# Optimization experiments

Hardware: AMD Instinct MI355X
Metric: run time of the kernel (lower is better)

The kernel has to match this reference:

```python
import jax, jax.numpy as jnp
import numpy as np

R_MIN = 0.01
R_MAX = 0.6
H = 32            # polar radial bins (after pooling)
W = 64            # polar angular bins (after pooling)
UP_R = 10         # radial upsampling factor
UP_T = 10         # angular upsampling factor
ATT_ALPHA = 5.0
B, C, IMG = 64, 3, 224


def _conv(x, w, b):
    # NCHW valid conv, stride 1 (matches nn.Conv2d default padding=0)
    y = jax.lax.conv_general_dilated(x, w, (1, 1), 'VALID',
                                     dimension_numbers=('NCHW', 'OIHW', 'NCHW'))
    return y + b[None, :, None, None]


def _maxpool2(x):
    return jax.lax.reduce_window(x, -jnp.inf, jax.lax.max,
                                 (1, 1, 2, 2), (1, 1, 2, 2), 'VALID')


def _grid_sample_border(x, grid):
    # F.grid_sample, bilinear, padding_mode='border', align_corners=False
    Bn, Cn, Hi, Wi = x.shape
    ix = ((grid[..., 0] + 1.0) * Wi - 1.0) * 0.5   # x-coord -> width index
    iy = ((grid[..., 1] + 1.0) * Hi - 1.0) * 0.5   # y-coord -> height index
    x0f = jnp.floor(ix)
    y0f = jnp.floor(iy)
    wx = (ix - x0f)[..., None]
    wy = (iy - y0f)[..., None]
    x0 = jnp.clip(x0f.astype(jnp.int32), 0, Wi - 1)
    x1 = jnp.clip(x0f.astype(jnp.int32) + 1, 0, Wi - 1)
    y0 = jnp.clip(y0f.astype(jnp.int32), 0, Hi - 1)
    y1 = jnp.clip(y0f.astype(jnp.int32) + 1, 0, Hi - 1)
    bidx = jnp.arange(Bn)[:, None, None]
    v00 = x[bidx, :, y0, x0]   # [B,Hg,Wg,C]
    v01 = x[bidx, :, y0, x1]
    v10 = x[bidx, :, y1, x0]
    v11 = x[bidx, :, y1, x1]
    out = (v00 * (1 - wx) * (1 - wy) + v01 * wx * (1 - wy)
           + v10 * (1 - wx) * wy + v11 * wx * wy)
    return jnp.transpose(out, (0, 3, 1, 2))  # [B,C,Hg,Wg]


def setup_inputs() -> dict:
    key = jax.random.key(0)
    ks = jax.random.split(key, 10)
    x = jax.random.normal(ks[0], (B, C, IMG, IMG), dtype=jnp.float32)
    l_t_prev = jax.random.uniform(ks[1], (B, 2), dtype=jnp.float32)
    conv1_w = jax.random.normal(ks[2], (6, C, 5, 5), dtype=jnp.float32) * 0.1
    conv1_b = jnp.zeros((6,), jnp.float32)
    conv2_w = jax.random.normal(ks[3], (16, 6, 5, 5), dtype=jnp.float32) * 0.1
    conv2_b = jnp.zeros((16,), jnp.float32)
    fc1_w = jax.random.normal(ks[4], (8, 16), dtype=jnp.float32) * 0.1
    fc1_b = jnp.zeros((8,), jnp.float32)
    fc2_w = jax.random.normal(ks[5], (2, 8), dtype=jnp.float32) * 0.1
    fc2_b = jnp.zeros((2,), jnp.float32)
    return dict(x=x, l_t_prev=l_t_prev, conv1_w=conv1_w, conv1_b=conv1_b,
                conv2_w=conv2_w, conv2_b=conv2_b, fc1_w=fc1_w, fc1_b=fc1_b,
                fc2_w=fc2_w, fc2_b=fc2_b)


def reference(x, l_t_prev, conv1_w, conv1_b, conv2_w, conv2_b,
              fc1_w, fc1_b, fc2_w, fc2_b):
    # --- attention branch: conv -> maxpool -> conv -> GAP -> fc -> sigmoid ---
    h = _conv(x, conv1_w, conv1_b)
    h = _maxpool2(h)
    h = _conv(h, conv2_w, conv2_b)
    feat = h.mean(axis=(2, 3))                     # AdaptiveAvgPool2d(1), [B,16]
    h = jax.nn.relu(feat @ fc1_w.T + fc1_b)
    weight = jax.nn.sigmoid(h @ fc2_w.T + fc2_b) * ATT_ALPHA   # [B,2]
    # --- per-batch log-polar grid ---
    Hg, Wg = H * UP_R, W * UP_T
    angle = 2.0 * jnp.pi * jnp.arange(Wg, dtype=jnp.float32) / Wg
    unit = jnp.stack([jnp.sin(angle), jnp.cos(angle)], axis=-1)   # [Wg,2]
    start = jnp.log(R_MIN * weight[:, 0])
    stop = jnp.log(R_MAX * weight[:, 1])
    t = jnp.arange(Hg, dtype=jnp.float32) / (Hg - 1)
    radii = jnp.exp(start[:, None] + (stop - start)[:, None] * t[None])  # [B,Hg]
    grid = radii[:, :, None, None] * unit[None, None]     # [B,Hg,Wg,2]
    grid = grid + l_t_prev[:, None, None, :]
    # --- irregular bilinear sampling + box filter ---
    sampled = _grid_sample_border(x, grid)                 # [B,C,Hg,Wg]
    Bn, Cn = sampled.shape[:2]
    pooled = sampled.reshape(Bn, Cn, H, UP_R, W, UP_T).mean(axis=(3, 5))
    return pooled, weight
```

## Files before the change

kernel.cpp:

```cpp
#include <hip/hip_runtime.h>
#include <math.h>

#define Bn    64
#define Cn    3
#define IMG   224
#define PLANE (IMG*IMG)
#define C1    6
#define P1    110
#define NVALID (106*106)
#define Hh    32
#define Ww    64
#define UPR   10
#define UPT   10
#define Hg    (Hh*UPR)
#define Wg    (Ww*UPT)
#define POOLED_SIZE (Bn*Cn*Hh*Ww)
#define NCHUNK 28
#define PSTRIDE 152
#define ROWB  (IMG*8)
#define TPB1  448

typedef unsigned short u16;
typedef unsigned long long ull;
typedef _Float16 h8v __attribute__((ext_vector_type(8)));
typedef float f4v __attribute__((ext_vector_type(4)));

#define PART_FLOATS ((size_t)Bn * NCHUNK * PSTRIDE)
#define X4B_U16     ((size_t)Bn * PLANE * 4)
#define WS_NEEDED   ((PART_FLOATS + Bn * 2) * 4 + X4B_U16 * 2)

__device__ __forceinline__ unsigned hpack(float a, float b) {
    union { _Float16 h; u16 u; } x, y;
    x.h = (_Float16)a; y.h = (_Float16)b;
    return (unsigned)x.u | ((unsigned)y.u << 16);
}
__device__ __forceinline__ float h2lo(unsigned v) {
    union { _Float16 h; u16 u; } c; c.u = (u16)(v & 0xffffu); return (float)c.h;
}
__device__ __forceinline__ float h2hi(unsigned v) {
    union { _Float16 h; u16 u; } c; c.u = (u16)(v >> 16); return (float)c.h;
}

#define GSHFL(v, idx) __shfl((v), (lane & 48) + (idx), 64)

__global__ __launch_bounds__(TPB1) void k1_fused(
    const float* __restrict__ x,
    const float* __restrict__ w1,
    const float* __restrict__ b1,
    float* __restrict__ partial,
    u16* __restrict__ x4h,
    int do_pack)
{
    __shared__ __attribute__((aligned(16))) unsigned char xs[12 * ROWB + 128];
    __shared__ __attribute__((aligned(16))) _Float16 sa[5][64][8];
    __shared__ float rowR[7][C1][4];
    __shared__ float edgeLo[4][C1][4];
    __shared__ float edgeHi[4][C1][4];

    const int b     = blockIdx.x;
    const int chunk = blockIdx.y;
    const int tid   = threadIdx.x;
    const int wid   = tid >> 6;
    const int lane  = tid & 63;
    const int n     = lane & 15;
    const int g     = lane >> 4;
    const int gy0   = chunk * 8;

    const float* xb = x + (size_t)b * (Cn * PLANE);
    u16* ob = x4h + (size_t)b * PLANE * 4;

    if (wid == 0) {
        #pragma unroll
        for (int ky = 0; ky < 5; ++ky) {
            #pragma unroll
            for (int j = 0; j < 8; ++j) {
                const int kmem = g * 8 + j;
                const int ic = kmem & 3, kx = kmem >> 2;
                float w = 0.0f;
                if (n < C1 && ic < 3 && kx < 5)
                    w = w1[((n * 3 + ic) * 5 + ky) * 5 + kx];
                sa[ky][lane][j] = (_Float16)w;
            }
        }
    } else {
        for (int i = tid - 64; i < 12 * 112; i += TPB1 - 64) {
            const int r = i / 112;
            const int p = i - r * 112;
            const int gy = gy0 + r;
            uint4 U; U.x = U.y = U.z = U.w = 0u;
            if (gy < IMG) {
                const float2 v0 = *(const float2*)(xb + 0 * PLANE + gy * IMG + 2 * p);
                const float2 v1 = *(const float2*)(xb + 1 * PLANE + gy * IMG + 2 * p);
                const float2 v2 = *(const float2*)(xb + 2 * PLANE + gy * IMG + 2 * p);
                U.x = hpack(v0.x, v1.x);
                U.y = hpack(v2.x, 0.0f);
                U.z = hpack(v0.y, v1.y);
                U.w = hpack(v2.y, 0.0f);
            }
            *(uint4*)(xs + r * ROWB + p * 16) = U;
            if (do_pack && r < 8)
                *(uint4*)(ob + ((size_t)gy * IMG + 2 * p) * 4) = U;
        }
    }
    __syncthreads();

    h8v a[5];
    #pragma unroll
    for (int ky = 0; ky < 5; ++ky) a[ky] = *(const h8v*)&sa[ky][lane][0];
    f4v binit;
    #pragma unroll
    for (int e = 0; e < 4; ++e) {
        const int oc = g * 4 + e;
        binit[e] = (oc < C1) ? b1[oc] : 0.0f;
    }

    float colsum[4][4];
    #pragma unroll
    for (int py = 0; py < 4; ++py)
        #pragma unroll
        for (int e = 0; e < 4; ++e) colsum[py][e] = 0.0f;

    #pragma unroll
    for (int si = 0; si < 2; ++si) {
        const int s = wid * 2 + si;
        const unsigned sByte = (unsigned)(s * 128 + n * 8 + g * 16);

        f4v acc[8];
        #pragma unroll
        for (int q = 0; q < 8; ++q) acc[q] = binit;

        #pragma unroll
        for (int r = 0; r < 12; ++r) {
            h8v bf;
            const unsigned char* bp = xs + r * ROWB + sByte;
            ((ull*)&bf)[0] = *(const ull*)bp;
            ((ull*)&bf)[1] = *(const ull*)(bp + 8);
            #pragma unroll
            for (int ky = 0; ky < 5; ++ky) {
                const int q = r - ky;
                if (q >= 0 && q < 8)
                    acc[q] = __builtin_amdgcn_mfma_f32_16x16x32_f16(
                        a[ky], bf, acc[q], 0, 0, 0);
            }
        }

        #pragma unroll
        for (int py = 0; py < 4; ++py) {
            #pragma unroll
            for (int e = 0; e < 4; ++e) {
                float t = fmaxf(acc[2 * py][e], acc[2 * py + 1][e]);
                t = fmaxf(t, __shfl_xor(t, 1, 64));
                if (s == 13 && n >= 12) t = 0.0f;
                colsum[py][e] += t;
                const int oc = g * 4 + e;
                if (s == 0) {
                    const float c0 = GSHFL(t, 0), c1 = GSHFL(t, 2);
                    const float c2 = GSHFL(t, 4), c3 = GSHFL(t, 6);
                    const float S1 = c0, S2 = S1 + c1, S3 = S2 + c2, S4 = S3 + c3;
                    const float sv = (n == 0) ? S1 : (n == 1) ? S2 : (n == 2) ? S3 : S4;
                    if (n < 4 && oc < C1) edgeLo[py][oc][n] = sv;
                }
                if (s == 13) {
                    const float d109 = GSHFL(t, 10), d108 = GSHFL(t, 8);
                    const float d107 = GSHFL(t, 6),  d106 = GSHFL(t, 4);
                    const float U1 = d109, U2 = U1 + d108, U3 = U2 + d107, U4 = U3 + d106;
                    const float uv = (n == 0) ? U1 : (n == 1) ? U2 : (n == 2) ? U3 : U4;
                    if (n < 4 && oc < C1) edgeHi[py][oc][n] = uv;
                }
            }
        }
    }

    #pragma unroll
    for (int py = 0; py < 4; ++py) {
        #pragma unroll
        for (int e = 0; e < 4; ++e) {
            float v = colsum[py][e];
            v += __shfl_xor(v, 2, 64);
            v += __shfl_xor(v, 4, 64);
            v += __shfl_xor(v, 8, 64);
            const int oc = g * 4 + e;
            if (n == 0 && oc < C1) rowR[wid][oc][py] = v;
        }
    }
    __syncthreads();

    if (tid < 150) {
        const int oc = tid / 25;
        const int rem = tid - oc * 25;
        const int ky = rem / 5, kx = rem - ky * 5;
        float total = 0.0f;
        #pragma unroll
        for (int py = 0; py < 4; ++py) {
            const int y = chunk * 4 + py;
            const bool valid = (y < P1) && ((unsigned)(y - ky) <= 105u);
            float v = rowR[0][oc][py] + rowR[1][oc][py] + rowR[2][oc][py]
                    + rowR[3][oc][py] + rowR[4][oc][py] + rowR[5][oc][py]
                    + rowR[6][oc][py];
            if (kx > 0) v -= edgeLo[py][oc][kx - 1];
            if (kx < 4) v -= edgeHi[py][oc][3 - kx];
            total += valid ? v : 0.0f;
        }
        partial[((size_t)b * NCHUNK + chunk) * PSTRIDE + tid] = total;
    }
}

__global__ __launch_bounds__(256) void k2_head(
    const float* __restrict__ partial, const float* __restrict__ w2,
    const float* __restrict__ b2, const float* __restrict__ fc1w,
    const float* __restrict__ fc1b, const float* __restrict__ fc2w,
    const float* __restrict__ fc2b, float* __restrict__ wt_ws,
    float* __restrict__ out)
{
    const int b = blockIdx.x;
    const int tid = threadIdx.x;
    __shared__ float wsb[150];
    __shared__ float sfeat[16];
    __shared__ float sh[8];

    if (tid < 150) {
        const float* p = partial + (size_t)b * NCHUNK * PSTRIDE + tid;
        float s = 0.0f;
        #pragma unroll
        for (int c = 0; c < NCHUNK; ++c) s += p[c * PSTRIDE];
        wsb[tid] = s;
    }
    __syncthreads();
    if (tid < 16) {
        float s = 0.0f;
        for (int j = 0; j < 150; ++j) s += w2[tid * 150 + j] * wsb[j];
        sfeat[tid] = b2[tid] + s * (1.0f / (float)NVALID);
    }
    __syncthreads();
    if (tid < 8) {
        float s = fc1b[tid];
        #pragma unroll
        for (int j = 0; j < 16; ++j) s += fc1w[tid * 16 + j] * sfeat[j];
        sh[tid] = fmaxf(s, 0.0f);
    }
    __syncthreads();
    if (tid < 2) {
        float s = fc2b[tid];
        #pragma unroll
        for (int j = 0; j < 8; ++j) s += fc2w[tid * 8 + j] * sh[j];
        float sig = (s >= 0.0f) ? (1.0f / (1.0f + expf(-s)))
                                : (expf(s) / (1.0f + expf(s)));
        const float wgt = 5.0f * sig;
        wt_ws[b * 2 + tid] = wgt;
        out[POOLED_SIZE + b * 2 + tid] = wgt;
    }
}

__device__ __forceinline__ void sample_coords(
    float gxn, float gyn, int& x0, int& y0, float& wx, float& wy)
{
    float ix = ((gxn + 1.0f) * (float)IMG - 1.0f) * 0.5f;
    float iy = ((gyn + 1.0f) * (float)IMG - 1.0f) * 0.5f;
    ix = fminf(fmaxf(ix, 0.0f), (float)(IMG - 1));
    iy = fminf(fmaxf(iy, 0.0f), (float)(IMG - 1));
    x0 = (int)ix; if (x0 > IMG - 2) x0 = IMG - 2;
    y0 = (int)iy; if (y0 > IMG - 2) y0 = IMG - 2;
    wx = ix - (float)x0;
    wy = iy - (float)y0;
}

__global__ __launch_bounds__(640) void k3_fused_head(
    const u16* __restrict__ x4h,
    const float* __restrict__ ltp,
    const float* __restrict__ partial,
    const float* __restrict__ w2,  const float* __restrict__ b2,
    const float* __restrict__ fc1w, const float* __restrict__ fc1b,
    const float* __restrict__ fc2w, const float* __restrict__ fc2b,
    float* __restrict__ out)
{
    __shared__ float part[3 * Wg];
    __shared__ float wsb[152];
    __shared__ float sfp[16][10];
    __shared__ float sfeat[16];
    __shared__ float sh[8];
    __shared__ float sWt[2];

    const int L = blockIdx.x;
    const int q = L >> 3;
    const int h = q & 31;
    const int b = (L & 7) + 8 * (q >> 5);
    const int tid = threadIdx.x;

    if (tid < 150) {
        const float* p = partial + (size_t)b * NCHUNK * PSTRIDE + tid;
        float s = 0.0f;
        #pragma unroll
        for (int c = 0; c < NCHUNK; ++c) s += p[c * PSTRIDE];
        wsb[tid] = s;
    }
    __syncthreads();
    if (tid < 160) {
        const int oc = tid / 10, gq = tid - (tid / 10) * 10;
        float s = 0.0f;
        #pragma unroll
        for (int j = 0; j < 15; ++j)
            s += w2[oc * 150 + gq * 15 + j] * wsb[gq * 15 + j];
        sfp[oc][gq] = s;
    }
    __syncthreads();
    if (tid < 16) {
        float s = 0.0f;
        #pragma unroll
        for (int g2 = 0; g2 < 10; ++g2) s += sfp[tid][g2];
        sfeat[tid] = b2[tid] + s * (1.0f / (float)NVALID);
    }
    __syncthreads();
    if (tid < 8) {
        float s = fc1b[tid];
        #pragma unroll
        for (int j = 0; j < 16; ++j) s += fc1w[tid * 16 + j] * sfeat[j];
        sh[tid] = fmaxf(s, 0.0f);
    }
    __syncthreads();
    if (tid < 2) {
        float s = fc2b[tid];
        #pragma unroll
        for (int j = 0; j < 8; ++j) s += fc2w[tid * 8 + j] * sh[j];
        const float sig = (s >= 0.0f) ? (1.0f / (1.0f + expf(-s)))
                                      : (expf(s) / (1.0f + expf(s)));
        const float wgt = 5.0f * sig;
        sWt[tid] = wgt;
        if (h == 0) out[POOLED_SIZE + b * 2 + tid] = wgt;
    }
    __syncthreads();

    const float w0 = sWt[0];
    const float w1 = sWt[1];
    const float l0 = ltp[b * 2 + 0];
    const float l1 = ltp[b * 2 + 1];
    const float start = logf(0.01f * w0);
    const float stop  = logf(0.6f  * w1);
    const float dr = stop - start;

    const float angle = 6.283185307179586f * (float)tid / (float)Wg;
    const float sn = __sinf(angle);
    const float cs = __cosf(angle);

    const u16* xb4 = x4h + (size_t)b * PLANE * 4;

    int xi[UPR], yi[UPR];
    float wxa[UPR], wya[UPR];
    #pragma unroll
    for (int i = 0; i < UPR; ++i) {
        const float ri = __expf(start + dr * ((float)(h * UPR + i)
                                              * (1.0f / (float)(Hg - 1))));
        sample_coords(ri * sn + l0, ri * cs + l1, xi[i], yi[i], wxa[i], wya[i]);
    }

    float acc0 = 0.0f, acc1 = 0.0f, acc2 = 0.0f;
    #pragma unroll
    for (int bb = 0; bb < 2; ++bb) {
        uint4 R0[5], R1[5];
        #pragma unroll
        for (int i = 0; i < 5; ++i) {
            const int s = bb * 5 + i;
            const u16* base = xb4 + ((size_t)(yi[s] * IMG + xi[s])) * 4;
            R0[i] = *(const uint4*)(base);
            R1[i] = *(const uint4*)(base + IMG * 4);
        }
        #pragma unroll
        for (int i = 0; i < 5; ++i) {
            const int s = bb * 5 + i;
            const float wx = wxa[s], wy = wya[s];
            const float wx0 = 1.0f - wx, wy0 = 1.0f - wy;
            const float w00 = wx0 * wy0, w01 = wx * wy0;
            const float w10 = wx0 * wy,  w11 = wx * wy;
            acc0 += w00*h2lo(R0[i].x) + w01*h2lo(R0[i].z)
                  + w10*h2lo(R1[i].x) + w11*h2lo(R1[i].z);
            acc1 += w00*h2hi(R0[i].x) + w01*h2hi(R0[i].z)
                  + w10*h2hi(R1[i].x) + w11*h2hi(R1[i].z);
            acc2 += w00*h2lo(R0[i].y) + w01*h2lo(R0[i].w)
                  + w10*h2lo(R1[i].y) + w11*h2lo(R1[i].w);
        }
    }
    part[0 * Wg + tid] = acc0;
    part[1 * Wg + tid] = acc1;
    part[2 * Wg + tid] = acc2;
    __syncthreads();

    if (tid < Cn * Ww) {
        const int c = tid / Ww;
        const int w = tid % Ww;
        const float* p = part + c * Wg + w * UPT;
        float s = 0.0f;
        #pragma unroll
        for (int j = 0; j < UPT; ++j) s += p[j];
        out[(((size_t)b * Cn + c) * Hh + h) * Ww + w] = s * (1.0f / (UPR * UPT));
    }
}

__global__ __launch_bounds__(640) void k3_sample_pool_nchw(
    const float* __restrict__ x, const float* __restrict__ ltp,
    const float* __restrict__ wt, float* __restrict__ out)
{
    __shared__ float part[3 * Wg];
    const int L = blockIdx.x;
    const int q = L >> 3;
    const int h = q & 31;
    const int b = (L & 7) + 8 * (q >> 5);
    const int tid = threadIdx.x;

    const float w0 = wt[b * 2 + 0];
    const float w1 = wt[b * 2 + 1];
    const float l0 = ltp[b * 2 + 0];
    const float l1 = ltp[b * 2 + 1];
    const float start = logf(0.01f * w0);
    const float stop  = logf(0.6f  * w1);
    const float dr = stop - start;
    const float angle = 6.283185307179586f * (float)tid / (float)Wg;
    const float sn = __sinf(angle);
    const float cs = __cosf(angle);
    const float* xb = x + (size_t)b * Cn * PLANE;

    float acc0 = 0.0f, acc1 = 0.0f, acc2 = 0.0f;
    #pragma unroll
    for (int i = 0; i < UPR; ++i) {
        const float ri = __expf(start + dr * ((float)(h * UPR + i)
                                              * (1.0f / (float)(Hg - 1))));
        int x0, y0; float wx, wy;
        sample_coords(ri * sn + l0, ri * cs + l1, x0, y0, wx, wy);
        const float wx0 = 1.0f - wx, wy0 = 1.0f - wy;
        const float w00 = wx0 * wy0, w01 = wx * wy0;
        const float w10 = wx0 * wy,  w11 = wx * wy;
        const int o00 = y0 * IMG + x0;
        acc0 += w00*xb[o00] + w01*xb[o00+1] + w10*xb[o00+IMG] + w11*xb[o00+IMG+1];
        const float* x1p = xb + PLANE;
        acc1 += w00*x1p[o00] + w01*x1p[o00+1] + w10*x1p[o00+IMG] + w11*x1p[o00+IMG+1];
        const float* x2p = xb + 2 * PLANE;
        acc2 += w00*x2p[o00] + w01*x2p[o00+1] + w10*x2p[o00+IMG] + w11*x2p[o00+IMG+1];
    }
    part[0 * Wg + tid] = acc0;
    part[1 * Wg + tid] = acc1;
    part[2 * Wg + tid] = acc2;
    __syncthreads();

    if (tid < Cn * Ww) {
        const int c = tid / Ww;
        const int w = tid % Ww;
        const float* p = part + c * Wg + w * UPT;
        float s = 0.0f;
        #pragma unroll
        for (int j = 0; j < UPT; ++j) s += p[j];
        out[(((size_t)b * Cn + c) * Hh + h) * Ww + w] = s * (1.0f / (UPR * UPT));
    }
}

extern "C" void kernel_launch(void* const* d_in, const int* in_sizes, int n_in,
                              void* d_out, int out_size, void* d_ws, size_t ws_size,
                              hipStream_t stream) {
    const float* x       = (const float*)d_in[0];
    const float* ltp     = (const float*)d_in[1];
    const float* conv1_w = (const float*)d_in[2];
    const float* conv1_b = (const float*)d_in[3];
    const float* conv2_w = (const float*)d_in[4];
    const float* conv2_b = (const float*)d_in[5];
    const float* fc1_w   = (const float*)d_in[6];
    const float* fc1_b   = (const float*)d_in[7];
    const float* fc2_w   = (const float*)d_in[8];
    const float* fc2_b   = (const float*)d_in[9];
    float* out = (float*)d_out;

    const int do_pack = (ws_size >= WS_NEEDED) ? 1 : 0;

    float* part_ws = (float*)d_ws;
    float* wt_ws   = part_ws + PART_FLOATS;
    u16*   x4h     = (u16*)(wt_ws + Bn * 2);

    k1_fused<<<dim3(Bn, NCHUNK), dim3(TPB1), 0, stream>>>(
        x, conv1_w, conv1_b, part_ws, x4h, do_pack);

    if (do_pack) {
        k3_fused_head<<<dim3(Hh * Bn), dim3(Wg), 0, stream>>>(
            x4h, ltp, part_ws, conv2_w, conv2_b,
            fc1_w, fc1_b, fc2_w, fc2_b, out);
    } else {
        k2_head<<<dim3(Bn), dim3(256), 0, stream>>>(part_ws, conv2_w, conv2_b,
                                                    fc1_w, fc1_b, fc2_w, fc2_b,
                                                    wt_ws, out);
        k3_sample_pool_nchw<<<dim3(Hh * Bn), dim3(Wg), 0, stream>>>(
            x, ltp, wt_ws, out);
    }
}
```

Baseline: 174.3 us.

## Split conv1 into small 2D-tiled single-wave blocks with atomic accumulation

Replaces the 448-thread per-row-chunk conv kernel with 64-thread blocks that each own a 16x16 spatial tile (14x14 tiles per image), staging the fp16-packed tile in a small shared buffer. Per-block window sums are accumulated into a single per-batch buffer with atomicAdd, so the head kernels no longer reduce over 28 partial chunks. A new single-block prep kernel builds the fp16 MFMA weight fragments once and zeroes the accumulator. The aim is more parallelism and less shared memory per block. The cost is an extra launch, halo rows loaded twice by neighbouring tiles, atomic contention, and float summation order that is no longer deterministic.

```diff
diff --git a/kernel.cpp b/kernel.cpp
--- a/kernel.cpp
+++ b/kernel.cpp
@@ -15,24 +15,29 @@
 #define Hg    (Hh*UPR)
 #define Wg    (Ww*UPT)
 #define POOLED_SIZE (Bn*Cn*Hh*Ww)
-#define NCHUNK 28
-#define PSTRIDE 152
-#define ROWB  (IMG*8)
-#define TPB1  448
+#define WSTRIDE 152
+
+#define NSTRIP 14
+#define NCP    14
+#define NBLK1  (NSTRIP*NCP*Bn)
+#define XROW   24
+#define NROW   20
 
 typedef unsigned short u16;
 typedef unsigned long long ull;
 typedef _Float16 h8v __attribute__((ext_vector_type(8)));
 typedef float f4v __attribute__((ext_vector_type(4)));
 
-#define PART_FLOATS ((size_t)Bn * NCHUNK * PSTRIDE)
-#define X4B_U16     ((size_t)Bn * PLANE * 4)
-#define WS_NEEDED   ((PART_FLOATS + Bn * 2) * 4 + X4B_U16 * 2)
-
-__device__ __forceinline__ unsigned hpack(float a, float b) {
-    union { _Float16 h; u16 u; } x, y;
-    x.h = (_Float16)a; y.h = (_Float16)b;
-    return (unsigned)x.u | ((unsigned)y.u << 16);
+#define WSUM_F   ((size_t)Bn * WSTRIDE)
+#define WT_OFF   WSUM_F
+#define AF_OFF_F (WSUM_F + Bn*2)
+#define AF_U16   (5*64*8)
+#define X4H_OFF_F (AF_OFF_F + AF_U16/2)
+#define X4B_U16  ((size_t)Bn * PLANE * 4)
+#define WS_NEEDED ((size_t)X4H_OFF_F * 4 + X4B_U16 * 2)
+
+__device__ __forceinline__ u16 f16b(float f) {
+    union { _Float16 h; u16 u; } c; c.h = (_Float16)f; return c.u;
 }
 __device__ __forceinline__ float h2lo(unsigned v) {
     union { _Float16 h; u16 u; } c; c.u = (u16)(v & 0xffffu); return (float)c.h;
@@ -43,87 +48,98 @@
 
 #define GSHFL(v, idx) __shfl((v), (lane & 48) + (idx), 64)
 
-__global__ __launch_bounds__(TPB1) void k1_fused(
-    const float* __restrict__ x,
-    const float* __restrict__ w1,
-    const float* __restrict__ b1,
-    float* __restrict__ partial,
-    u16* __restrict__ x4h,
-    int do_pack)
-{
-    __shared__ __attribute__((aligned(16))) unsigned char xs[12 * ROWB + 128];
-    __shared__ __attribute__((aligned(16))) _Float16 sa[5][64][8];
-    __shared__ float rowR[7][C1][4];
-    __shared__ float edgeLo[4][C1][4];
-    __shared__ float edgeHi[4][C1][4];
-
-    const int b     = blockIdx.x;
-    const int chunk = blockIdx.y;
-    const int tid   = threadIdx.x;
-    const int wid   = tid >> 6;
-    const int lane  = tid & 63;
-    const int n     = lane & 15;
-    const int g     = lane >> 4;
-    const int gy0   = chunk * 8;
-
-    const float* xb = x + (size_t)b * (Cn * PLANE);
-    u16* ob = x4h + (size_t)b * PLANE * 4;
-
-    if (wid == 0) {
+__global__ __launch_bounds__(256) void k0_prep(
+    const float* __restrict__ w1, u16* __restrict__ af,
+    float* __restrict__ wsum)
+{
+    const int tid = threadIdx.x;
+    if (tid < 64) {
+        const int n = tid & 15, g = tid >> 4;
         #pragma unroll
         for (int ky = 0; ky < 5; ++ky) {
             #pragma unroll
             for (int j = 0; j < 8; ++j) {
-                const int kmem = g * 8 + j;
-                const int ic = kmem & 3, kx = kmem >> 2;
+                const int k = g * 8 + j, ic = k & 3, kx = k >> 2;
                 float w = 0.0f;
                 if (n < C1 && ic < 3 && kx < 5)
                     w = w1[((n * 3 + ic) * 5 + ky) * 5 + kx];
-                sa[ky][lane][j] = (_Float16)w;
+                af[(ky * 64 + tid) * 8 + j] = f16b(w);
             }
         }
-    } else {
-        for (int i = tid - 64; i < 12 * 112; i += TPB1 - 64) {
-            const int r = i / 112;
-            const int p = i - r * 112;
-            const int gy = gy0 + r;
-            uint4 U; U.x = U.y = U.z = U.w = 0u;
-            if (gy < IMG) {
-                const float2 v0 = *(const float2*)(xb + 0 * PLANE + gy * IMG + 2 * p);
-                const float2 v1 = *(const float2*)(xb + 1 * PLANE + gy * IMG + 2 * p);
-                const float2 v2 = *(const float2*)(xb + 2 * PLANE + gy * IMG + 2 * p);
-                U.x = hpack(v0.x, v1.x);
-                U.y = hpack(v2.x, 0.0f);
-                U.z = hpack(v0.y, v1.y);
-                U.w = hpack(v2.y, 0.0f);
-            }
-            *(uint4*)(xs + r * ROWB + p * 16) = U;
-            if (do_pack && r < 8)
-                *(uint4*)(ob + ((size_t)gy * IMG + 2 * p) * 4) = U;
-        }
-    }
-    __syncthreads();
+    }
+    for (int i = tid; i < Bn * WSTRIDE; i += 256) wsum[i] = 0.0f;
+}
+
+__global__ __launch_bounds__(64) void k1_conv(
+    const float* __restrict__ x,
+    const u16*   __restrict__ af,
+    const float* __restrict__ b1f,
+    float* __restrict__ wsum,
+    u16* __restrict__ x4h,
+    int do_pack)
+{
+    __shared__ __attribute__((aligned(16))) u16 xs[NROW][XROW * 4];
+    __shared__ float sc[C1][4];
+    __shared__ float eL[C1][4][4];
+    __shared__ float eH[C1][4][4];
+
+    const int L    = blockIdx.x;
+    const int b    = L & 63;
+    const int z    = L >> 6;
+    const int cp   = z / NSTRIP;
+    const int s    = z - cp * NSTRIP;
+    const int gy0  = cp * 16;
+    const int gx0  = s * 16;
+    const int lane = threadIdx.x;
+    const int n    = lane & 15;
+    const int g    = lane >> 4;
+
+    const float* xb = x + (size_t)b * (Cn * PLANE);
+
+    for (int i = lane; i < NROW * 3 * 6; i += 64) {
+        const int r   = i / 18;
+        const int rem = i - r * 18;
+        const int ch  = rem / 6;
+        const int qd  = rem - ch * 6;
+        const int gy  = gy0 + r;
+        const int gx  = gx0 + qd * 4;
+        float4 v; v.x = v.y = v.z = v.w = 0.0f;
+        if (gy < IMG && gx + 3 < IMG)
+            v = *(const float4*)(xb + ch * PLANE + gy * IMG + gx);
+        u16* d = &xs[r][qd * 16 + ch];
+        d[0]  = f16b(v.x);
+        d[4]  = f16b(v.y);
+        d[8]  = f16b(v.z);
+        d[12] = f16b(v.w);
+    }
 
     h8v a[5];
     #pragma unroll
-    for (int ky = 0; ky < 5; ++ky) a[ky] = *(const h8v*)&sa[ky][lane][0];
+    for (int ky = 0; ky < 5; ++ky)
+        a[ky] = *(const h8v*)(af + (ky * 64 + lane) * 8);
     f4v binit;
     #pragma unroll
     for (int e = 0; e < 4; ++e) {
         const int oc = g * 4 + e;
-        binit[e] = (oc < C1) ? b1[oc] : 0.0f;
-    }
-
-    float colsum[4][4];
-    #pragma unroll
-    for (int py = 0; py < 4; ++py)
-        #pragma unroll
-        for (int e = 0; e < 4; ++e) colsum[py][e] = 0.0f;
-
-    #pragma unroll
-    for (int si = 0; si < 2; ++si) {
-        const int s = wid * 2 + si;
-        const unsigned sByte = (unsigned)(s * 128 + n * 8 + g * 16);
+        binit[e] = (oc < C1) ? b1f[oc] : 0.0f;
+    }
+
+    __syncthreads();
+
+    if (do_pack) {
+        const int row = lane >> 3, pp = lane & 7;
+        u16* ob = x4h + (size_t)b * PLANE * 4;
+        #pragma unroll
+        for (int h2 = 0; h2 < 2; ++h2) {
+            const int rr = row + h2 * 8;
+            const int gy = gy0 + rr;
+            const uint4 v = *(const uint4*)&xs[rr][pp * 8];
+            *(uint4*)(ob + ((size_t)gy * IMG + gx0 + pp * 2) * 4) = v;
+        }
+    }
+
+    for (int chh = 0; chh < 2; ++chh) {
+        const int chunk = cp * 2 + chh;
 
         f4v acc[8];
         #pragma unroll
@@ -131,10 +147,10 @@
 
         #pragma unroll
         for (int r = 0; r < 12; ++r) {
+            const u16* bp = &xs[chh * 8 + r][(n + 2 * g) * 4];
             h8v bf;
-            const unsigned char* bp = xs + r * ROWB + sByte;
             ((ull*)&bf)[0] = *(const ull*)bp;
-            ((ull*)&bf)[1] = *(const ull*)(bp + 8);
+            ((ull*)&bf)[1] = *(const ull*)(bp + 4);
             #pragma unroll
             for (int ky = 0; ky < 5; ++ky) {
                 const int q = r - ky;
@@ -150,63 +166,58 @@
             for (int e = 0; e < 4; ++e) {
                 float t = fmaxf(acc[2 * py][e], acc[2 * py + 1][e]);
                 t = fmaxf(t, __shfl_xor(t, 1, 64));
-                if (s == 13 && n >= 12) t = 0.0f;
-                colsum[py][e] += t;
+                if (s == NSTRIP - 1 && n >= 12) t = 0.0f;
                 const int oc = g * 4 + e;
                 if (s == 0) {
                     const float c0 = GSHFL(t, 0), c1 = GSHFL(t, 2);
                     const float c2 = GSHFL(t, 4), c3 = GSHFL(t, 6);
                     const float S1 = c0, S2 = S1 + c1, S3 = S2 + c2, S4 = S3 + c3;
-                    const float sv = (n == 0) ? S1 : (n == 1) ? S2 : (n == 2) ? S3 : S4;
-                    if (n < 4 && oc < C1) edgeLo[py][oc][n] = sv;
+                    const float sv = (n == 0) ? S1 : (n == 1) ? S2
+                                   : (n == 2) ? S3 : S4;
+                    if (n < 4 && oc < C1) eL[oc][py][n] = sv;
                 }
-                if (s == 13) {
+                if (s == NSTRIP - 1) {
                     const float d109 = GSHFL(t, 10), d108 = GSHFL(t, 8);
                     const float d107 = GSHFL(t, 6),  d106 = GSHFL(t, 4);
-                    const float U1 = d109, U2 = U1 + d108, U3 = U2 + d107, U4 = U3 + d106;
-                    const float uv = (n == 0) ? U1 : (n == 1) ? U2 : (n == 2) ? U3 : U4;
-                    if (n < 4 && oc < C1) edgeHi[py][oc][n] = uv;
+                    const float U1 = d109, U2 = U1 + d108, U3 = U2 + d107,
+                                U4 = U3 + d106;
+                    const float uv = (n == 0) ? U1 : (n == 1) ? U2
+                                   : (n == 2) ? U3 : U4;
+                    if (n < 4 && oc < C1) eH[oc][py][n] = uv;
+                }
+                float v = t;
+                v += __shfl_xor(v, 2, 64);
+                v += __shfl_xor(v, 4, 64);
+                v += __shfl_xor(v, 8, 64);
+                if (n == 0 && oc < C1) sc[oc][py] = v;
+            }
+        }
+        __syncthreads();
+
+        for (int t0 = lane; t0 < 150; t0 += 64) {
+            const int oc  = t0 / 25;
+            const int rem = t0 - oc * 25;
+            const int ky  = rem / 5, kx = rem - ky * 5;
+            float total = 0.0f;
+            #pragma unroll
+            for (int py = 0; py < 4; ++py) {
+                const int y = chunk * 4 + py;
+                const bool valid = (y < P1) && ((unsigned)(y - ky) <= 105u);
+                if (valid) {
+                    float v = sc[oc][py];
+                    if (s == 0 && kx > 0)          v -= eL[oc][py][kx - 1];
+                    if (s == NSTRIP - 1 && kx < 4) v -= eH[oc][py][3 - kx];
+                    total += v;
                 }
             }
-        }
-    }
-
-    #pragma unroll
-    for (int py = 0; py < 4; ++py) {
-        #pragma unroll
-        for (int e = 0; e < 4; ++e) {
-            float v = colsum[py][e];
-            v += __shfl_xor(v, 2, 64);
-            v += __shfl_xor(v, 4, 64);
-            v += __shfl_xor(v, 8, 64);
-            const int oc = g * 4 + e;
-            if (n == 0 && oc < C1) rowR[wid][oc][py] = v;
-        }
-    }
-    __syncthreads();
-
-    if (tid < 150) {
-        const int oc = tid / 25;
-        const int rem = tid - oc * 25;
-        const int ky = rem / 5, kx = rem - ky * 5;
-        float total = 0.0f;
-        #pragma unroll
-        for (int py = 0; py < 4; ++py) {
-            const int y = chunk * 4 + py;
-            const bool valid = (y < P1) && ((unsigned)(y - ky) <= 105u);
-            float v = rowR[0][oc][py] + rowR[1][oc][py] + rowR[2][oc][py]
-                    + rowR[3][oc][py] + rowR[4][oc][py] + rowR[5][oc][py]
-                    + rowR[6][oc][py];
-            if (kx > 0) v -= edgeLo[py][oc][kx - 1];
-            if (kx < 4) v -= edgeHi[py][oc][3 - kx];
-            total += valid ? v : 0.0f;
-        }
-        partial[((size_t)b * NCHUNK + chunk) * PSTRIDE + tid] = total;
+            atomicAdd(&wsum[b * WSTRIDE + t0], total);
+        }
+        __syncthreads();
     }
 }
 
 __global__ __launch_bounds__(256) void k2_head(
-    const float* __restrict__ partial, const float* __restrict__ w2,
+    const float* __restrict__ wsum, const float* __restrict__ w2,
     const float* __restrict__ b2, const float* __restrict__ fc1w,
     const float* __restrict__ fc1b, const float* __restrict__ fc2w,
     const float* __restrict__ fc2b, float* __restrict__ wt_ws,
@@ -218,13 +229,7 @@
     __shared__ float sfeat[16];
     __shared__ float sh[8];
 
-    if (tid < 150) {
-        const float* p = partial + (size_t)b * NCHUNK * PSTRIDE + tid;
-        float s = 0.0f;
-        #pragma unroll
-        for (int c = 0; c < NCHUNK; ++c) s += p[c * PSTRIDE];
-        wsb[tid] = s;
-    }
+    if (tid < 150) wsb[tid] = wsum[b * WSTRIDE + tid];
     __syncthreads();
     if (tid < 16) {
         float s = 0.0f;
@@ -267,7 +272,7 @@
 __global__ __launch_bounds__(640) void k3_fused_head(
     const u16* __restrict__ x4h,
     const float* __restrict__ ltp,
-    const float* __restrict__ partial,
+    const float* __restrict__ wsum,
     const float* __restrict__ w2,  const float* __restrict__ b2,
     const float* __restrict__ fc1w, const float* __restrict__ fc1b,
     const float* __restrict__ fc2w, const float* __restrict__ fc2b,
@@ -286,13 +291,7 @@
     const int b = (L & 7) + 8 * (q >> 5);
     const int tid = threadIdx.x;
 
-    if (tid < 150) {
-        const float* p = partial + (size_t)b * NCHUNK * PSTRIDE + tid;
-        float s = 0.0f;
-        #pragma unroll
-        for (int c = 0; c < NCHUNK; ++c) s += p[c * PSTRIDE];
-        wsb[tid] = s;
-    }
+    if (tid < 150) wsb[tid] = wsum[b * WSTRIDE + tid];
     __syncthreads();
     if (tid < 160) {
         const int oc = tid / 10, gq = tid - (tid / 10) * 10;
@@ -358,15 +357,15 @@
         uint4 R0[5], R1[5];
         #pragma unroll
         for (int i = 0; i < 5; ++i) {
-            const int s = bb * 5 + i;
-            const u16* base = xb4 + ((size_t)(yi[s] * IMG + xi[s])) * 4;
+            const int sI = bb * 5 + i;
+            const u16* base = xb4 + ((size_t)(yi[sI] * IMG + xi[sI])) * 4;
             R0[i] = *(const uint4*)(base);
             R1[i] = *(const uint4*)(base + IMG * 4);
         }
         #pragma unroll
         for (int i = 0; i < 5; ++i) {
-            const int s = bb * 5 + i;
-            const float wx = wxa[s], wy = wya[s];
+            const int sI = bb * 5 + i;
+            const float wx = wxa[sI], wy = wya[sI];
             const float wx0 = 1.0f - wx, wy0 = 1.0f - wy;
             const float w00 = wx0 * wy0, w01 = wx * wy0;
             const float w10 = wx0 * wy,  w11 = wx * wy;
@@ -467,19 +466,22 @@
 
     const int do_pack = (ws_size >= WS_NEEDED) ? 1 : 0;
 
-    float* part_ws = (float*)d_ws;
-    float* wt_ws   = part_ws + PART_FLOATS;
-    u16*   x4h     = (u16*)(wt_ws + Bn * 2);
-
-    k1_fused<<<dim3(Bn, NCHUNK), dim3(TPB1), 0, stream>>>(
-        x, conv1_w, conv1_b, part_ws, x4h, do_pack);
+    float* wsum  = (float*)d_ws;
+    float* wt_ws = wsum + WT_OFF;
+    u16*   af    = (u16*)(wsum + AF_OFF_F);
+    u16*   x4h   = (u16*)(wsum + X4H_OFF_F);
+
+    k0_prep<<<dim3(1), dim3(256), 0, stream>>>(conv1_w, af, wsum);
+
+    k1_conv<<<dim3(NBLK1), dim3(64), 0, stream>>>(
+        x, af, conv1_b, wsum, x4h, do_pack);
 
     if (do_pack) {
         k3_fused_head<<<dim3(Hh * Bn), dim3(Wg), 0, stream>>>(
-            x4h, ltp, part_ws, conv2_w, conv2_b,
+            x4h, ltp, wsum, conv2_w, conv2_b,
             fc1_w, fc1_b, fc2_w, fc2_b, out);
     } else {
-        k2_head<<<dim3(Bn), dim3(256), 0, stream>>>(part_ws, conv2_w, conv2_b,
+        k2_head<<<dim3(Bn), dim3(256), 0, stream>>>(wsum, conv2_w, conv2_b,
                                                     fc1_w, fc1_b, fc2_w, fc2_b,
                                                     wt_ws, out);
         k3_sample_pool_nchw<<<dim3(Hh * Bn), dim3(Wg), 0, stream>>>(
```

Result: slower. 188.2 us (+8.0%).

## Split fused conv kernel into pack, weight-prep and LDS-direct conv kernels

Applied to the files above, without the earlier changes.

The fused conv kernel, which packed fp32 NCHW input to fp16 channel-interleaved form and ran the MFMA conv in the same pass, is split into three kernels. A standalone pack kernel converts the whole input, a tiny kernel pre-packs the conv1 weights into fp16 MFMA fragments, and the conv kernel loads packed rows straight into LDS with global_load_lds. The aim is to shrink the conv kernel's prologue and its redundant per-block fp32 reads. The cost is two extra launches and an extra global round trip of the packed tensor before the conv can start.

```diff
diff --git a/kernel.cpp b/kernel.cpp
--- a/kernel.cpp
+++ b/kernel.cpp
@@ -21,19 +21,25 @@
 #define TPB1  448
 
 typedef unsigned short u16;
+typedef unsigned int u32;
 typedef unsigned long long ull;
 typedef _Float16 h8v __attribute__((ext_vector_type(8)));
 typedef float f4v __attribute__((ext_vector_type(4)));
 
 #define PART_FLOATS ((size_t)Bn * NCHUNK * PSTRIDE)
+#define AF_OFF_F    (PART_FLOATS + Bn * 2)
+#define X4H_OFF_F   (AF_OFF_F + 1280)
 #define X4B_U16     ((size_t)Bn * PLANE * 4)
-#define WS_NEEDED   ((PART_FLOATS + Bn * 2) * 4 + X4B_U16 * 2)
+#define WS_NEEDED   ((size_t)X4H_OFF_F * 4 + X4B_U16 * 2)
 
 __device__ __forceinline__ unsigned hpack(float a, float b) {
     union { _Float16 h; u16 u; } x, y;
     x.h = (_Float16)a; y.h = (_Float16)b;
     return (unsigned)x.u | ((unsigned)y.u << 16);
 }
+__device__ __forceinline__ u16 f16b(float f) {
+    union { _Float16 h; u16 u; } c; c.h = (_Float16)f; return c.u;
+}
 __device__ __forceinline__ float h2lo(unsigned v) {
     union { _Float16 h; u16 u; } c; c.u = (u16)(v & 0xffffu); return (float)c.h;
 }
@@ -43,16 +49,51 @@
 
 #define GSHFL(v, idx) __shfl((v), (lane & 48) + (idx), 64)
 
-__global__ __launch_bounds__(TPB1) void k1_fused(
-    const float* __restrict__ x,
-    const float* __restrict__ w1,
-    const float* __restrict__ b1,
-    float* __restrict__ partial,
-    u16* __restrict__ x4h,
-    int do_pack)
-{
-    __shared__ __attribute__((aligned(16))) unsigned char xs[12 * ROWB + 128];
-    __shared__ __attribute__((aligned(16))) _Float16 sa[5][64][8];
+__global__ __launch_bounds__(64) void k0_prep(
+    const float* __restrict__ w1, u16* __restrict__ af)
+{
+    const int tid = threadIdx.x;
+    const int n = tid & 15, g = tid >> 4;
+    #pragma unroll
+    for (int ky = 0; ky < 5; ++ky) {
+        #pragma unroll
+        for (int j = 0; j < 8; ++j) {
+            const int k = g * 8 + j, ic = k & 3, kx = k >> 2;
+            float w = 0.0f;
+            if (n < C1 && ic < 3 && kx < 5)
+                w = w1[((n * 3 + ic) * 5 + ky) * 5 + kx];
+            af[(ky * 64 + tid) * 8 + j] = f16b(w);
+        }
+    }
+}
+
+__global__ __launch_bounds__(256) void kA_pack(
+    const float* __restrict__ x, u16* __restrict__ x4h)
+{
+    const int i = blockIdx.x * 256 + threadIdx.x;
+    const int b  = i / (PLANE / 4);
+    const int p4 = i - b * (PLANE / 4);
+    const float* xb = x + (size_t)b * 3 * PLANE + p4 * 4;
+    const float4 c0 = *(const float4*)(xb);
+    const float4 c1 = *(const float4*)(xb + PLANE);
+    const float4 c2 = *(const float4*)(xb + 2 * PLANE);
+    uint4 W0, W1;
+    W0.x = hpack(c0.x, c1.x);  W0.y = hpack(c2.x, 0.0f);
+    W0.z = hpack(c0.y, c1.y);  W0.w = hpack(c2.y, 0.0f);
+    W1.x = hpack(c0.z, c1.z);  W1.y = hpack(c2.z, 0.0f);
+    W1.z = hpack(c0.w, c1.w);  W1.w = hpack(c2.w, 0.0f);
+    u16* ob = x4h + ((size_t)b * PLANE + p4 * 4) * 4;
+    *(uint4*)(ob)     = W0;
+    *(uint4*)(ob + 8) = W1;
+}
+
+__global__ __launch_bounds__(TPB1) void kB_conv(
+    const u16* __restrict__ x4h,
+    const u16* __restrict__ af,
+    const float* __restrict__ b1f,
+    float* __restrict__ partial)
+{
+    __shared__ __attribute__((aligned(16))) unsigned char xs[12 * ROWB];
     __shared__ float rowR[7][C1][4];
     __shared__ float edgeLo[4][C1][4];
     __shared__ float edgeHi[4][C1][4];
@@ -66,8 +107,295 @@
     const int g     = lane >> 4;
     const int gy0   = chunk * 8;
 
+    const int nInst = (chunk == NCHUNK - 1) ? 14 : 21;
+    if (chunk == NCHUNK - 1)
+        *(uint4*)(xs + 8 * ROWB + tid * 16) = (uint4){0u, 0u, 0u, 0u};
+
+    {
+        const char* gbase = (const char*)x4h
+                          + ((size_t)b * PLANE + (size_t)gy0 * IMG) * 8;
+        #pragma unroll
+        for (int k = 0; k < 3; ++k) {
+            const int j = wid * 3 + k;
+            if (j < nInst) {
+                const char* gp = gbase + j * 1024 + lane * 16;
+                __builtin_amdgcn_global_load_lds(
+                    (const __attribute__((address_space(1))) u32*)gp,
+                    (__attribute__((address_space(3))) u32*)(xs + j * 1024),
+                    16, 0, 0);
+            }
+        }
+    }
+
+    h8v a[5];
+    #pragma unroll
+    for (int ky = 0; ky < 5; ++ky)
+        a[ky] = *(const h8v*)(af + (ky * 64 + lane) * 8);
+    f4v binit;
+    #pragma unroll
+    for (int e = 0; e < 4; ++e) {
+        const int oc = g * 4 + e;
+        binit[e] = (oc < C1) ? b1f[oc] : 0.0f;
+    }
+
+    __syncthreads();
+
+    float colsum[4][4];
+    #pragma unroll
+    for (int py = 0; py < 4; ++py)
+        #pragma unroll
+        for (int e = 0; e < 4; ++e) colsum[py][e] = 0.0f;
+
+    #pragma unroll
+    for (int si = 0; si < 2; ++si) {
+        const int s = wid * 2 + si;
+        const unsigned sByte = (unsigned)(s * 128 + n * 8 + g * 16);
+
+        f4v acc[8];
+        #pragma unroll
+        for (int q = 0; q < 8; ++q) acc[q] = binit;
+
+        #pragma unroll
+        for (int r = 0; r < 12; ++r) {
+            h8v bf;
+            const unsigned char* bp = xs + r * ROWB + sByte;
+            ((ull*)&bf)[0] = *(const ull*)bp;
+            ((ull*)&bf)[1] = *(const ull*)(bp + 8);
+            #pragma unroll
+            for (int ky = 0; ky < 5; ++ky) {
+                const int q = r - ky;
+                if (q >= 0 && q < 8)
+                    acc[q] = __builtin_amdgcn_mfma_f32_16x16x32_f16(
+                        a[ky], bf, acc[q], 0, 0, 0);
+            }
+        }
+
+        #pragma unroll
+        for (int py = 0; py < 4; ++py) {
+            #pragma unroll
+            for (int e = 0; e < 4; ++e) {
+                float t = fmaxf(acc[2 * py][e], acc[2 * py + 1][e]);
+                t = fmaxf(t, __shfl_xor(t, 1, 64));
+                if (s == 13 && n >= 12) t = 0.0f;
+                colsum[py][e] += t;
+                const int oc = g * 4 + e;
+                if (s == 0) {
+                    const float c0 = GSHFL(t, 0), c1 = GSHFL(t, 2);
+                    const float c2 = GSHFL(t, 4), c3 = GSHFL(t, 6);
+                    const float S1 = c0, S2 = S1 + c1, S3 = S2 + c2, S4 = S3 + c3;
+                    const float sv = (n == 0) ? S1 : (n == 1) ? S2
+                                   : (n == 2) ? S3 : S4;
+                    if (n < 4 && oc < C1) edgeLo[py][oc][n] = sv;
+                }
+                if (s == 13) {
+                    const float d109 = GSHFL(t, 10), d108 = GSHFL(t, 8);
+                    const float d107 = GSHFL(t, 6),  d106 = GSHFL(t, 4);
+                    const float U1 = d109, U2 = U1 + d108, U3 = U2 + d107,
+                                U4 = U3 + d106;
+                    const float uv = (n == 0) ? U1 : (n == 1) ? U2
+                                   : (n == 2) ? U3 : U4;
+                    if (n < 4 && oc < C1) edgeHi[py][oc][n] = uv;
+                }
+            }
+        }
+    }
+
+    #pragma unroll
+    for (int py = 0; py < 4; ++py) {
+        #pragma unroll
+        for (int e = 0; e < 4; ++e) {
+            float v = colsum[py][e];
+            v += __shfl_xor(v, 2, 64);
+            v += __shfl_xor(v, 4, 64);
+            v += __shfl_xor(v, 8, 64);
+            const int oc = g * 4 + e;
+            if (n == 0 && oc < C1) rowR[wid][oc][py] = v;
+        }
+    }
+    __syncthreads();
+
+    if (tid < 150) {
+        const int oc = tid / 25;
+        const int rem = tid - oc * 25;
+        const int ky = rem / 5, kx = rem - ky * 5;
+        float total = 0.0f;
+        #pragma unroll
+        for (int py = 0; py < 4; ++py) {
+            const int y = chunk * 4 + py;
+            const bool valid = (y < P1) && ((unsigned)(y - ky) <= 105u);
+            float v = rowR[0][oc][py] + rowR[1][oc][py] + rowR[2][oc][py]
+                    + rowR[3][oc][py] + rowR[4][oc][py] + rowR[5][oc][py]
+                    + rowR[6][oc][py];
+            if (kx > 0) v -= edgeLo[py][oc][kx - 1];
+            if (kx < 4) v -= edgeHi[py][oc][3 - kx];
+            total += valid ? v : 0.0f;
+        }
+        partial[((size_t)b * NCHUNK + chunk) * PSTRIDE + tid] = total;
+    }
+}
+
+__device__ __forceinline__ void sample_coords(
+    float gxn, float gyn, int& x0, int& y0, float& wx, float& wy)
+{
+    float ix = ((gxn + 1.0f) * (float)IMG - 1.0f) * 0.5f;
+    float iy = ((gyn + 1.0f) * (float)IMG - 1.0f) * 0.5f;
+    ix = fminf(fmaxf(ix, 0.0f), (float)(IMG - 1));
+    iy = fminf(fmaxf(iy, 0.0f), (float)(IMG - 1));
+    x0 = (int)ix; if (x0 > IMG - 2) x0 = IMG - 2;
+    y0 = (int)iy; if (y0 > IMG - 2) y0 = IMG - 2;
+    wx = ix - (float)x0;
+    wy = iy - (float)y0;
+}
+
+__global__ __launch_bounds__(640) void k3_fused_head(
+    const u16* __restrict__ x4h,
+    const float* __restrict__ ltp,
+    const float* __restrict__ partial,
+    const float* __restrict__ w2,  const float* __restrict__ b2,
+    const float* __restrict__ fc1w, const float* __restrict__ fc1b,
+    const float* __restrict__ fc2w, const float* __restrict__ fc2b,
+    float* __restrict__ out)
+{
+    __shared__ float part[3 * Wg];
+    __shared__ float wsb[152];
+    __shared__ float sfp[16][10];
+    __shared__ float sfeat[16];
+    __shared__ float sh[8];
+    __shared__ float sWt[2];
+
+    const int L = blockIdx.x;
+    const int q = L >> 3;
+    const int h = q & 31;
+    const int b = (L & 7) + 8 * (q >> 5);
+    const int tid = threadIdx.x;
+
+    if (tid < 150) {
+        const float* p = partial + (size_t)b * NCHUNK * PSTRIDE + tid;
+        float s = 0.0f;
+        #pragma unroll
+        for (int c = 0; c < NCHUNK; ++c) s += p[c * PSTRIDE];
+        wsb[tid] = s;
+    }
+    __syncthreads();
+    if (tid < 160) {
+        const int oc = tid / 10, gq = tid - (tid / 10) * 10;
+        float s = 0.0f;
+        #pragma unroll
+        for (int j = 0; j < 15; ++j)
+            s += w2[oc * 150 + gq * 15 + j] * wsb[gq * 15 + j];
+        sfp[oc][gq] = s;
+    }
+    __syncthreads();
+    if (tid < 16) {
+        float s = 0.0f;
+        #pragma unroll
+        for (int g2 = 0; g2 < 10; ++g2) s += sfp[tid][g2];
+        sfeat[tid] = b2[tid] + s * (1.0f / (float)NVALID);
+    }
+    __syncthreads();
+    if (tid < 8) {
+        float s = fc1b[tid];
+        #pragma unroll
+        for (int j = 0; j < 16; ++j) s += fc1w[tid * 16 + j] * sfeat[j];
+        sh[tid] = fmaxf(s, 0.0f);
+    }
+    __syncthreads();
+    if (tid < 2) {
+        float s = fc2b[tid];
+        #pragma unroll
+        for (int j = 0; j < 8; ++j) s += fc2w[tid * 8 + j] * sh[j];
+        const float sig = (s >= 0.0f) ? (1.0f / (1.0f + expf(-s)))
+                                      : (expf(s) / (1.0f + expf(s)));
+        const float wgt = 5.0f * sig;
+        sWt[tid] = wgt;
+        if (h == 0) out[POOLED_SIZE + b * 2 + tid] = wgt;
+    }
+    __syncthreads();
+
+    const float w0 = sWt[0];
+    const float w1 = sWt[1];
+    const float l0 = ltp[b * 2 + 0];
+    const float l1 = ltp[b * 2 + 1];
+    const float start = logf(0.01f * w0);
+    const float stop  = logf(0.6f  * w1);
+    const float dr = stop - start;
+
+    const float angle = 6.283185307179586f * (float)tid / (float)Wg;
+    const float sn = __sinf(angle);
+    const float cs = __cosf(angle);
+
+    const u16* xb4 = x4h + (size_t)b * PLANE * 4;
+
+    int xi[UPR], yi[UPR];
+    float wxa[UPR], wya[UPR];
+    #pragma unroll
+    for (int i = 0; i < UPR; ++i) {
+        const float ri = __expf(start + dr * ((float)(h * UPR + i)
+                                              * (1.0f / (float)(Hg - 1))));
+        sample_coords(ri * sn + l0, ri * cs + l1, xi[i], yi[i], wxa[i], wya[i]);
+    }
+
+    float acc0 = 0.0f, acc1 = 0.0f, acc2 = 0.0f;
+    #pragma unroll
+    for (int bb = 0; bb < 2; ++bb) {
+        uint4 R0[5], R1[5];
+        #pragma unroll
+        for (int i = 0; i < 5; ++i) {
+            const int sI = bb * 5 + i;
+            const u16* base = xb4 + ((size_t)(yi[sI] * IMG + xi[sI])) * 4;
+            R0[i] = *(const uint4*)(base);
+            R1[i] = *(const uint4*)(base + IMG * 4);
+        }
+        #pragma unroll
+        for (int i = 0; i < 5; ++i) {
+            const int sI = bb * 5 + i;
+            const float wx = wxa[sI], wy = wya[sI];
+            const float wx0 = 1.0f - wx, wy0 = 1.0f - wy;
+            const float w00 = wx0 * wy0, w01 = wx * wy0;
+            const float w10 = wx0 * wy,  w11 = wx * wy;
+            acc0 += w00*h2lo(R0[i].x) + w01*h2lo(R0[i].z)
+                  + w10*h2lo(R1[i].x) + w11*h2lo(R1[i].z);
+            acc1 += w00*h2hi(R0[i].x) + w01*h2hi(R0[i].z)
+                  + w10*h2hi(R1[i].x) + w11*h2hi(R1[i].z);
+            acc2 += w00*h2lo(R0[i].y) + w01*h2lo(R0[i].w)
+                  + w10*h2lo(R1[i].y) + w11*h2lo(R1[i].w);
+        }
+    }
+    part[0 * Wg + tid] = acc0;
+    part[1 * Wg + tid] = acc1;
+    part[2 * Wg + tid] = acc2;
+    __syncthreads();
+
+    if (tid < Cn * Ww) {
+        const int c = tid / Ww;
+        const int w = tid % Ww;
+        const float* p = part + c * Wg + w * UPT;
+        float s = 0.0f;
+        #pragma unroll
+        for (int j = 0; j < UPT; ++j) s += p[j];
+        out[(((size_t)b * Cn + c) * Hh + h) * Ww + w] = s * (1.0f / (UPR * UPT));
+    }
+}
+
+__global__ __launch_bounds__(TPB1) void k1_legacy(
+    const float* __restrict__ x, const float* __restrict__ w1,
+    const float* __restrict__ b1, float* __restrict__ partial)
+{
+    __shared__ __attribute__((aligned(16))) unsigned char xs[12 * ROWB + 128];
+    __shared__ __attribute__((aligned(16))) _Float16 sa[5][64][8];
+    __shared__ float rowR[7][C1][4];
+    __shared__ float edgeLo[4][C1][4];
+    __shared__ float edgeHi[4][C1][4];
+
+    const int b     = blockIdx.x;
+    const int chunk = blockIdx.y;
+    const int tid   = threadIdx.x;
+    const int wid   = tid >> 6;
+    const int lane  = tid & 63;
+    const int n     = lane & 15;
+    const int g     = lane >> 4;
+    const int gy0   = chunk * 8;
     const float* xb = x + (size_t)b * (Cn * PLANE);
-    u16* ob = x4h + (size_t)b * PLANE * 4;
 
     if (wid == 0) {
         #pragma unroll
@@ -98,8 +426,6 @@
                 U.w = hpack(v2.y, 0.0f);
             }
             *(uint4*)(xs + r * ROWB + p * 16) = U;
-            if (do_pack && r < 8)
-                *(uint4*)(ob + ((size_t)gy * IMG + 2 * p) * 4) = U;
         }
     }
     __syncthreads();
@@ -124,11 +450,9 @@
     for (int si = 0; si < 2; ++si) {
         const int s = wid * 2 + si;
         const unsigned sByte = (unsigned)(s * 128 + n * 8 + g * 16);
-
         f4v acc[8];
         #pragma unroll
         for (int q = 0; q < 8; ++q) acc[q] = binit;
-
         #pragma unroll
         for (int r = 0; r < 12; ++r) {
             h8v bf;
@@ -143,7 +467,6 @@
                         a[ky], bf, acc[q], 0, 0, 0);
             }
         }
-
         #pragma unroll
         for (int py = 0; py < 4; ++py) {
             #pragma unroll
@@ -157,20 +480,22 @@
                     const float c0 = GSHFL(t, 0), c1 = GSHFL(t, 2);
                     const float c2 = GSHFL(t, 4), c3 = GSHFL(t, 6);
                     const float S1 = c0, S2 = S1 + c1, S3 = S2 + c2, S4 = S3 + c3;
-                    const float sv = (n == 0) ? S1 : (n == 1) ? S2 : (n == 2) ? S3 : S4;
+                    const float sv = (n == 0) ? S1 : (n == 1) ? S2
+                                   : (n == 2) ? S3 : S4;
                     if (n < 4 && oc < C1) edgeLo[py][oc][n] = sv;
                 }
                 if (s == 13) {
                     const float d109 = GSHFL(t, 10), d108 = GSHFL(t, 8);
                     const float d107 = GSHFL(t, 6),  d106 = GSHFL(t, 4);
-                    const float U1 = d109, U2 = U1 + d108, U3 = U2 + d107, U4 = U3 + d106;
-                    const float uv = (n == 0) ? U1 : (n == 1) ? U2 : (n == 2) ? U3 : U4;
+                    const float U1 = d109, U2 = U1 + d108, U3 = U2 + d107,
+                                U4 = U3 + d106;
+                    const float uv = (n == 0) ? U1 : (n == 1) ? U2
+                                   : (n == 2) ? U3 : U4;
                     if (n < 4 && oc < C1) edgeHi[py][oc][n] = uv;
                 }
             }
         }
     }
-
     #pragma unroll
     for (int py = 0; py < 4; ++py) {
         #pragma unroll
@@ -184,7 +509,6 @@
         }
     }
     __syncthreads();
-
     if (tid < 150) {
         const int oc = tid / 25;
         const int rem = tid - oc * 25;
@@ -248,149 +572,6 @@
         const float wgt = 5.0f * sig;
         wt_ws[b * 2 + tid] = wgt;
         out[POOLED_SIZE + b * 2 + tid] = wgt;
-    }
-}
-
-__device__ __forceinline__ void sample_coords(
-    float gxn, float gyn, int& x0, int& y0, float& wx, float& wy)
-{
-    float ix = ((gxn + 1.0f) * (float)IMG - 1.0f) * 0.5f;
-    float iy = ((gyn + 1.0f) * (float)IMG - 1.0f) * 0.5f;
-    ix = fminf(fmaxf(ix, 0.0f), (float)(IMG - 1));
-    iy = fminf(fmaxf(iy, 0.0f), (float)(IMG - 1));
-    x0 = (int)ix; if (x0 > IMG - 2) x0 = IMG - 2;
-    y0 = (int)iy; if (y0 > IMG - 2) y0 = IMG - 2;
-    wx = ix - (float)x0;
-    wy = iy - (float)y0;
-}
-
-__global__ __launch_bounds__(640) void k3_fused_head(
-    const u16* __restrict__ x4h,
-    const float* __restrict__ ltp,
-    const float* __restrict__ partial,
-    const float* __restrict__ w2,  const float* __restrict__ b2,
-    const float* __restrict__ fc1w, const float* __restrict__ fc1b,
-    const float* __restrict__ fc2w, const float* __restrict__ fc2b,
-    float* __restrict__ out)
-{
-    __shared__ float part[3 * Wg];
-    __shared__ float wsb[152];
-    __shared__ float sfp[16][10];
-    __shared__ float sfeat[16];
-    __shared__ float sh[8];
-    __shared__ float sWt[2];
-
-    const int L = blockIdx.x;
-    const int q = L >> 3;
-    const int h = q & 31;
-    const int b = (L & 7) + 8 * (q >> 5);
-    const int tid = threadIdx.x;
-
-    if (tid < 150) {
-        const float* p = partial + (size_t)b * NCHUNK * PSTRIDE + tid;
-        float s = 0.0f;
-        #pragma unroll
-        for (int c = 0; c < NCHUNK; ++c) s += p[c * PSTRIDE];
-        wsb[tid] = s;
-    }
-    __syncthreads();
-    if (tid < 160) {
-        const int oc = tid / 10, gq = tid - (tid / 10) * 10;
-        float s = 0.0f;
-        #pragma unroll
-        for (int j = 0; j < 15; ++j)
-            s += w2[oc * 150 + gq * 15 + j] * wsb[gq * 15 + j];
-        sfp[oc][gq] = s;
-    }
-    __syncthreads();
-    if (tid < 16) {
-        float s = 0.0f;
-        #pragma unroll
-        for (int g2 = 0; g2 < 10; ++g2) s += sfp[tid][g2];
-        sfeat[tid] = b2[tid] + s * (1.0f / (float)NVALID);
-    }
-    __syncthreads();
-    if (tid < 8) {
-        float s = fc1b[tid];
-        #pragma unroll
-        for (int j = 0; j < 16; ++j) s += fc1w[tid * 16 + j] * sfeat[j];
-        sh[tid] = fmaxf(s, 0.0f);
-    }
-    __syncthreads();
-    if (tid < 2) {
-        float s = fc2b[tid];
-        #pragma unroll
-        for (int j = 0; j < 8; ++j) s += fc2w[tid * 8 + j] * sh[j];
-        const float sig = (s >= 0.0f) ? (1.0f / (1.0f + expf(-s)))
-                                      : (expf(s) / (1.0f + expf(s)));
-        const float wgt = 5.0f * sig;
-        sWt[tid] = wgt;
-        if (h == 0) out[POOLED_SIZE + b * 2 + tid] = wgt;
-    }
-    __syncthreads();
-
-    const float w0 = sWt[0];
-    const float w1 = sWt[1];
-    const float l0 = ltp[b * 2 + 0];
-    const float l1 = ltp[b * 2 + 1];
-    const float start = logf(0.01f * w0);
-    const float stop  = logf(0.6f  * w1);
-    const float dr = stop - start;
-
-    const float angle = 6.283185307179586f * (float)tid / (float)Wg;
-    const float sn = __sinf(angle);
-    const float cs = __cosf(angle);
-
-    const u16* xb4 = x4h + (size_t)b * PLANE * 4;
-
-    int xi[UPR], yi[UPR];
-    float wxa[UPR], wya[UPR];
-    #pragma unroll
-    for (int i = 0; i < UPR; ++i) {
-        const float ri = __expf(start + dr * ((float)(h * UPR + i)
-                                              * (1.0f / (float)(Hg - 1))));
-        sample_coords(ri * sn + l0, ri * cs + l1, xi[i], yi[i], wxa[i], wya[i]);
-    }
-
-    float acc0 = 0.0f, acc1 = 0.0f, acc2 = 0.0f;
-    #pragma unroll
-    for (int bb = 0; bb < 2; ++bb) {
-        uint4 R0[5], R1[5];
-        #pragma unroll
-        for (int i = 0; i < 5; ++i) {
-            const int s = bb * 5 + i;
-            const u16* base = xb4 + ((size_t)(yi[s] * IMG + xi[s])) * 4;
-            R0[i] = *(const uint4*)(base);
-            R1[i] = *(const uint4*)(base + IMG * 4);
-        }
-        #pragma unroll
-        for (int i = 0; i < 5; ++i) {
-            const int s = bb * 5 + i;
-            const float wx = wxa[s], wy = wya[s];
-            const float wx0 = 1.0f - wx, wy0 = 1.0f - wy;
-            const float w00 = wx0 * wy0, w01 = wx * wy0;
-            const float w10 = wx0 * wy,  w11 = wx * wy;
-            acc0 += w00*h2lo(R0[i].x) + w01*h2lo(R0[i].z)
-                  + w10*h2lo(R1[i].x) + w11*h2lo(R1[i].z);
-            acc1 += w00*h2hi(R0[i].x) + w01*h2hi(R0[i].z)
-                  + w10*h2hi(R1[i].x) + w11*h2hi(R1[i].z);
-            acc2 += w00*h2lo(R0[i].y) + w01*h2lo(R0[i].w)
-                  + w10*h2lo(R1[i].y) + w11*h2lo(R1[i].w);
-        }
-    }
-    part[0 * Wg + tid] = acc0;
-    part[1 * Wg + tid] = acc1;
-    part[2 * Wg + tid] = acc2;
-    __syncthreads();
-
-    if (tid < Cn * Ww) {
-        const int c = tid / Ww;
-        const int w = tid % Ww;
-        const float* p = part + c * Wg + w * UPT;
-        float s = 0.0f;
-        #pragma unroll
-        for (int j = 0; j < UPT; ++j) s += p[j];
-        out[(((size_t)b * Cn + c) * Hh + h) * Ww + w] = s * (1.0f / (UPR * UPT));
     }
 }
 
@@ -469,16 +650,20 @@
 
     float* part_ws = (float*)d_ws;
     float* wt_ws   = part_ws + PART_FLOATS;
-    u16*   x4h     = (u16*)(wt_ws + Bn * 2);
-
-    k1_fused<<<dim3(Bn, NCHUNK), dim3(TPB1), 0, stream>>>(
-        x, conv1_w, conv1_b, part_ws, x4h, do_pack);
+    u16*   af      = (u16*)(part_ws + AF_OFF_F);
+    u16*   x4h     = (u16*)(part_ws + X4H_OFF_F);
 
     if (do_pack) {
+        k0_prep<<<dim3(1), dim3(64), 0, stream>>>(conv1_w, af);
+        kA_pack<<<dim3(Bn * PLANE / 4 / 256), dim3(256), 0, stream>>>(x, x4h);
+        kB_conv<<<dim3(Bn, NCHUNK), dim3(TPB1), 0, stream>>>(
+            x4h, af, conv1_b, part_ws);
         k3_fused_head<<<dim3(Hh * Bn), dim3(Wg), 0, stream>>>(
             x4h, ltp, part_ws, conv2_w, conv2_b,
             fc1_w, fc1_b, fc2_w, fc2_b, out);
     } else {
+        k1_legacy<<<dim3(Bn, NCHUNK), dim3(TPB1), 0, stream>>>(
+            x, conv1_w, conv1_b, part_ws);
         k2_head<<<dim3(Bn), dim3(256), 0, stream>>>(part_ws, conv2_w, conv2_b,
                                                     fc1_w, fc1_b, fc2_w, fc2_b,
                                                     wt_ws, out);
```

Result: no change. 172.4 us (-1.1%).
